# Optimization experiments

Measured on AMD Instinct MI355X. Metric: run time of the kernel, lower is better.

Reference implementation:

```python
import jax, jax.numpy as jnp
import numpy as np


def setup_inputs() -> dict:
    key = jax.random.key(0)
    k1, k2 = jax.random.split(key)
    return {
        "embeddings": jax.random.normal(k1, (4, 768, 32, 32), dtype=jnp.float32),
        "database": jax.random.normal(k2, (20000, 768), dtype=jnp.float32),
        "k": 3,
        "out_h": 512,
        "out_w": 512,
    }


def reference(embeddings, database, k, out_h, out_w):
    # embeddings: [B, D, h, w]  (segmenter hidden state), database: [N, D]
    B, D, h, w = embeddings.shape
    # B x h x w x D -> B x (h*w) x D query layout, as in _get_ood_scores
    q = jnp.transpose(embeddings, (0, 2, 3, 1)).reshape(B, h * w, D)
    # squared Euclidean distances via (||q||^2 + ||x||^2 - 2 q.x)
    q2 = jnp.sum(q * q, axis=-1)[..., None]                 # [B, hw, 1]
    x2 = jnp.sum(database * database, axis=-1)[None, None]  # [1, 1, N]
    d2 = q2 + x2 - 2.0 * jnp.einsum("bqd,nd->bqn", q, database)
    dist = jnp.sqrt(jnp.maximum(d2, 1e-12))                 # [B, hw, N]
    # k smallest distances (sklearn kneighbors) then mean over neighbors
    neg_topk, _ = jax.lax.top_k(-dist, k)                   # [B, hw, k]
    ood = jnp.mean(-neg_topk, axis=-1).reshape(B, h, w)
    # F.interpolate(..., mode='bilinear', align_corners=False) == half-pixel bilinear
    ood_up = jax.image.resize(ood[:, None], (B, 1, out_h, out_w), method="bilinear")
    return ood_up
```

## Files before the change

kernel.cpp:

```cpp
#include <hip/hip_runtime.h>
#include <hip/hip_bf16.h>
#include <math.h>

constexpr int B    = 4;
constexpr int D    = 768;
constexpr int HW   = 1024;
constexpr int M    = B * HW;
constexpr int NDB  = 20000;
constexpr int NDBP = 20096;
constexpr int OUTH = 512;
constexpr int OUTW = 512;

constexpr int BM     = 128;
constexpr int BN     = 128;
constexpr int KSTEPS = D / 64;
constexpr int GSTEPS = KSTEPS / 2;
constexpr int NSPLIT = 32;
constexpr int NT2    = 157;
constexpr int STEPB  = BM * 64;

typedef int   i32x8  __attribute__((ext_vector_type(8)));
typedef float f32x16 __attribute__((ext_vector_type(16)));

__device__ __forceinline__ void insert3(float& t0, float& t1, float& t2, float d) {
    float a0 = fminf(d, t0);
    float b0 = fmaxf(d, t0);
    float a1 = fminf(b0, t1);
    float b1 = fmaxf(b0, t1);
    t0 = a0; t1 = a1;
    t2 = fminf(b1, t2);
}

__device__ __forceinline__ unsigned int pack4_fp8(float a, float b, float c, float d) {
    int v = __builtin_amdgcn_cvt_pk_fp8_f32(a, b, 0, false);
    v = __builtin_amdgcn_cvt_pk_fp8_f32(c, d, v, true);
    return (unsigned int)v;
}

__device__ __forceinline__ void gl_lds16(const unsigned char* g, unsigned char* l) {
    __builtin_amdgcn_global_load_lds(
        (const __attribute__((address_space(1))) void*)g,
        (__attribute__((address_space(3))) void*)l, 16, 0, 0);
}

__global__ __launch_bounds__(256) void db_convert(const float* __restrict__ db,
                                                  uint4* __restrict__ dbt8,
                                                  float* __restrict__ x2p) {
    __shared__ float part[512];
    const int tile = blockIdx.x;
    const int g    = blockIdx.y;
    const int t    = threadIdx.x;
    const int n0   = tile * BM;

    #pragma unroll
    for (int pass = 0; pass < 2; ++pass) {
        int idx = pass * 256 + t;
        int r  = idx & 31;
        int kc = (idx >> 5) & 1;
        int h2 = (idx >> 6) & 1;
        int rg = idx >> 7;
        int row = rg * 32 + r;
        int n = n0 + row;
        int kb = g * 64 + kc * 32 + h2 * 16;
        float4 v0 = make_float4(0.f, 0.f, 0.f, 0.f), v1 = v0, v2 = v0, v3 = v0;
        if (n < NDB) {
            const float4* p = (const float4*)(db + (size_t)n * D + kb);
            v0 = p[0]; v1 = p[1]; v2 = p[2]; v3 = p[3];
        }
        float ss = v0.x*v0.x + v0.y*v0.y + v0.z*v0.z + v0.w*v0.w
                 + v1.x*v1.x + v1.y*v1.y + v1.z*v1.z + v1.w*v1.w
                 + v2.x*v2.x + v2.y*v2.y + v2.z*v2.z + v2.w*v2.w
                 + v3.x*v3.x + v3.y*v3.y + v3.z*v3.z + v3.w*v3.w;
        uint4 o;
        o.x = pack4_fp8(v0.x, v0.y, v0.z, v0.w);
        o.y = pack4_fp8(v1.x, v1.y, v1.z, v1.w);
        o.z = pack4_fp8(v2.x, v2.y, v2.z, v2.w);
        o.w = pack4_fp8(v3.x, v3.y, v3.z, v3.w);
        dbt8[((size_t)tile * KSTEPS + g) * 512 + idx] = o;
        part[idx] = ss;
    }
    __syncthreads();
    if (t < 128) {
        int rg = t >> 5, r = t & 31;
        int base = rg * 128 + r;
        float s = part[base] + part[base + 32] + part[base + 64] + part[base + 96];
        x2p[((size_t)tile * KSTEPS + g) * 128 + t] = s;
    }
}

__global__ __launch_bounds__(256) void x2_reduce(const float* __restrict__ x2p,
                                                 float* __restrict__ x2) {
    int n = blockIdx.x * 256 + threadIdx.x;
    if (n >= NDBP) return;
    if (n >= NDB) { x2[n] = 1e30f; return; }
    const float* p = x2p + (size_t)(n >> 7) * KSTEPS * 128 + (n & 127);
    float s = 0.f;
    #pragma unroll
    for (int g = 0; g < KSTEPS; ++g) s += p[g * 128];
    x2[n] = s;
}

__global__ __launch_bounds__(256) void q_convert(const float* __restrict__ emb,
                                                 uint4* __restrict__ qbt8,
                                                 float* __restrict__ q2p) {
    __shared__ float part[512];
    const int qt = blockIdx.x;
    const int g  = blockIdx.y;
    const int t  = threadIdx.x;
    const int b  = qt >> 3;
    const int p0 = (qt & 7) * 128;

    #pragma unroll
    for (int pass = 0; pass < 2; ++pass) {
        int idx = pass * 256 + t;
        int r  = idx & 31;
        int kc = (idx >> 5) & 1;
        int h2 = (idx >> 6) & 1;
        int rg = idx >> 7;
        int prow = rg * 32 + r;
        int kb = g * 64 + kc * 32 + h2 * 16;
        const float* src = emb + ((size_t)b * D + kb) * HW + p0 + prow;
        float v[16];
        float ss = 0.f;
        #pragma unroll
        for (int j = 0; j < 16; ++j) {
            v[j] = src[(size_t)j * HW];
            ss = fmaf(v[j], v[j], ss);
        }
        uint4 o;
        o.x = pack4_fp8(-2.f*v[0],  -2.f*v[1],  -2.f*v[2],  -2.f*v[3]);
        o.y = pack4_fp8(-2.f*v[4],  -2.f*v[5],  -2.f*v[6],  -2.f*v[7]);
        o.z = pack4_fp8(-2.f*v[8],  -2.f*v[9],  -2.f*v[10], -2.f*v[11]);
        o.w = pack4_fp8(-2.f*v[12], -2.f*v[13], -2.f*v[14], -2.f*v[15]);
        qbt8[((size_t)qt * KSTEPS + g) * 512 + idx] = o;
        part[idx] = ss;
    }
    __syncthreads();
    if (t < 128) {
        int rg = t >> 5, r = t & 31;
        int base = rg * 128 + r;
        float s = part[base] + part[base + 32] + part[base + 64] + part[base + 96];
        q2p[((size_t)qt * KSTEPS + g) * 128 + t] = s;
    }
}

__global__ __launch_bounds__(256, 4) void gemm_topk(const unsigned char* __restrict__ dbt8,
                                                    const unsigned char* __restrict__ qbt8,
                                                    const float* __restrict__ x2g,
                                                    float* __restrict__ partials) {
    __shared__ __align__(16) unsigned char As[2 * STEPB];
    __shared__ __align__(16) unsigned char Bs[2 * STEPB];
    __shared__ float X2s[BM];
    __shared__ float red[2][BN][3];

    const int tid  = threadIdx.x;
    const int lane = tid & 63;
    const int w    = tid >> 6;
    const int wr   = w >> 1, wc = w & 1;
    const int h    = lane >> 5;
    const int l31  = lane & 31;

    const int bid   = blockIdx.x;
    const int xcd   = bid & 7;
    const int j     = bid >> 3;
    const int sp    = xcd + 8 * (j >> 5);
    const int qtile = j & 31;
    const int m0    = qtile * BN;

    const int afrag = (wr * 2) * 2048 + h * 512 + l31 * 16;
    const int bfrag = (wc * 2) * 2048 + h * 512 + l31 * 16;

    const int lb = lane * 16;
    const unsigned char* qstep0 = qbt8 + (size_t)qtile * KSTEPS * STEPB + w * 2048 + lb;

    float t0[2], t1[2], t2[2];
    #pragma unroll
    for (int jj = 0; jj < 2; ++jj) { t0[jj] = INFINITY; t1[jj] = INFINITY; t2[jj] = INFINITY; }

    for (int tile = sp; tile < NT2; tile += NSPLIT) {
        const int n0 = tile * BM;
        const unsigned char* astep = dbt8 + (size_t)tile * KSTEPS * STEPB + w * 2048 + lb;
        const unsigned char* bstep = qstep0;

        f32x16 acc[2][2];
        #pragma unroll
        for (int i = 0; i < 2; ++i)
            #pragma unroll
            for (int jj = 0; jj < 2; ++jj)
                #pragma unroll
                for (int r = 0; r < 16; ++r) acc[i][jj][r] = 0.f;

        for (int g2 = 0; g2 < GSTEPS; ++g2) {
            __syncthreads();
            gl_lds16(astep,                As + w * 2048);
            gl_lds16(astep + 1024,         As + w * 2048 + 1024);
            gl_lds16(astep + STEPB,        As + 8192 + w * 2048);
            gl_lds16(astep + STEPB + 1024, As + 8192 + w * 2048 + 1024);
            gl_lds16(bstep,                Bs + w * 2048);
            gl_lds16(bstep + 1024,         Bs + w * 2048 + 1024);
            gl_lds16(bstep + STEPB,        Bs + 8192 + w * 2048);
            gl_lds16(bstep + STEPB + 1024, Bs + 8192 + w * 2048 + 1024);
            if (g2 == 0 && tid < BM) X2s[tid] = x2g[n0 + tid];
            astep += 2 * STEPB;
            bstep += 2 * STEPB;
            __syncthreads();

            #pragma unroll
            for (int s = 0; s < 2; ++s) {
                i32x8 af[2], bf[2];
                #pragma unroll
                for (int i = 0; i < 2; ++i) {
                    int4 lo = *(const int4*)(As + s * 8192 + afrag + i * 2048);
                    int4 hi = *(const int4*)(As + s * 8192 + afrag + i * 2048 + 1024);
                    af[i] = (i32x8){lo.x, lo.y, lo.z, lo.w, hi.x, hi.y, hi.z, hi.w};
                }
                #pragma unroll
                for (int jj = 0; jj < 2; ++jj) {
                    int4 lo = *(const int4*)(Bs + s * 8192 + bfrag + jj * 2048);
                    int4 hi = *(const int4*)(Bs + s * 8192 + bfrag + jj * 2048 + 1024);
                    bf[jj] = (i32x8){lo.x, lo.y, lo.z, lo.w, hi.x, hi.y, hi.z, hi.w};
                }
                #pragma unroll
                for (int i = 0; i < 2; ++i)
                    #pragma unroll
                    for (int jj = 0; jj < 2; ++jj)
                        acc[i][jj] = __builtin_amdgcn_mfma_scale_f32_32x32x64_f8f6f4(
                            af[i], bf[jj], acc[i][jj], 0, 0,
                            0, 0x7f7f7f7f, 0, 0x7f7f7f7f);
            }
        }

        #pragma unroll
        for (int i = 0; i < 2; ++i) {
            #pragma unroll
            for (int rg2 = 0; rg2 < 4; ++rg2) {
                float4 xv = *(const float4*)&X2s[wr * 64 + i * 32 + rg2 * 8 + 4 * h];
                #pragma unroll
                for (int jj = 0; jj < 2; ++jj) {
                    #pragma unroll
                    for (int rr = 0; rr < 4; ++rr) {
                        float s = acc[i][jj][rg2 * 4 + rr] + ((const float*)&xv)[rr];
                        insert3(t0[jj], t1[jj], t2[jj], s);
                    }
                }
            }
        }
    }

    #pragma unroll
    for (int jj = 0; jj < 2; ++jj) {
        float o0 = __shfl_xor(t0[jj], 32);
        float o1 = __shfl_xor(t1[jj], 32);
        float o2 = __shfl_xor(t2[jj], 32);
        insert3(t0[jj], t1[jj], t2[jj], o0);
        insert3(t0[jj], t1[jj], t2[jj], o1);
        insert3(t0[jj], t1[jj], t2[jj], o2);
    }
    if (h == 0) {
        #pragma unroll
        for (int jj = 0; jj < 2; ++jj) {
            int col = wc * 64 + jj * 32 + l31;
            red[wr][col][0] = t0[jj];
            red[wr][col][1] = t1[jj];
            red[wr][col][2] = t2[jj];
        }
    }
    __syncthreads();
    if (tid < BN) {
        float a0 = red[0][tid][0], a1 = red[0][tid][1], a2 = red[0][tid][2];
        insert3(a0, a1, a2, red[1][tid][0]);
        insert3(a0, a1, a2, red[1][tid][1]);
        insert3(a0, a1, a2, red[1][tid][2]);
        float* dst = partials + ((size_t)(m0 + tid) * NSPLIT + sp) * 3;
        dst[0] = a0; dst[1] = a1; dst[2] = a2;
    }
}

__global__ __launch_bounds__(256) void merge_ood(const float* __restrict__ partials,
                                                 const float* __restrict__ q2p,
                                                 float* __restrict__ ood) {
    int m = blockIdx.x * 256 + threadIdx.x;
    if (m >= M) return;
    const float* pp = partials + (size_t)m * NSPLIT * 3;
    float a0 = INFINITY, a1 = INFINITY, a2 = INFINITY;
    #pragma unroll
    for (int j = 0; j < NSPLIT * 3; ++j) insert3(a0, a1, a2, pp[j]);
    const float* qp = q2p + (size_t)(m >> 7) * KSTEPS * 128 + (m & 127);
    float q = 0.f;
    #pragma unroll
    for (int g = 0; g < KSTEPS; ++g) q += qp[g * 128];
    float d0 = sqrtf(fmaxf(q + a0, 1e-12f));
    float d1 = sqrtf(fmaxf(q + a1, 1e-12f));
    float d2 = sqrtf(fmaxf(q + a2, 1e-12f));
    ood[m] = (d0 + d1 + d2) * (1.f / 3.f);
}

__global__ __launch_bounds__(256) void upsample(const float* __restrict__ ood,
                                                float* __restrict__ out) {
    int idx = blockIdx.x * 256 + threadIdx.x;
    int ox = idx & (OUTW - 1);
    int oy = (idx >> 9) & (OUTH - 1);
    int bb = idx >> 18;
    float sx = (ox + 0.5f) * (32.f / OUTW) - 0.5f;
    float sy = (oy + 0.5f) * (32.f / OUTH) - 0.5f;
    float fx = floorf(sx), fy = floorf(sy);
    float wx = sx - fx, wy = sy - fy;
    int x0 = max(0, min(31, (int)fx));
    int x1 = max(0, min(31, (int)fx + 1));
    int y0 = max(0, min(31, (int)fy));
    int y1 = max(0, min(31, (int)fy + 1));
    const float* src = ood + bb * 1024;
    float v00 = src[y0 * 32 + x0];
    float v01 = src[y0 * 32 + x1];
    float v10 = src[y1 * 32 + x0];
    float v11 = src[y1 * 32 + x1];
    float top = v00 + wx * (v01 - v00);
    float bot = v10 + wx * (v11 - v10);
    out[idx] = top + wy * (bot - top);
}

extern "C" void kernel_launch(void* const* d_in, const int* in_sizes, int n_in,
                              void* d_out, int out_size, void* d_ws, size_t ws_size,
                              hipStream_t stream) {
    const float* emb = (const float*)d_in[0];
    const float* db  = (const float*)d_in[1];
    float* out = (float*)d_out;

    char* ws = (char*)d_ws;
    unsigned char* dbt8 = (unsigned char*)ws;
    unsigned char* qbt8 = (unsigned char*)(ws + 15433728);
    float* x2       = (float*)(ws + 18579456);
    float* x2p      = (float*)(ws + 18659840);
    float* q2p      = (float*)(ws + 19624448);
    float* ood      = (float*)(ws + 19821056);
    float* partials = (float*)(ws + 19837440);

    db_convert<<<dim3(NT2, KSTEPS), 256, 0, stream>>>(db, (uint4*)dbt8, x2p);
    q_convert<<<dim3(32, KSTEPS), 256, 0, stream>>>(emb, (uint4*)qbt8, q2p);
    x2_reduce<<<(NDBP + 255) / 256, 256, 0, stream>>>(x2p, x2);
    gemm_topk<<<NSPLIT * 32, 256, 0, stream>>>(dbt8, qbt8, x2, partials);
    merge_ood<<<(M + 255) / 256, 256, 0, stream>>>(partials, q2p, ood);
    upsample<<<(B * OUTH * OUTW) / 256, 256, 0, stream>>>(ood, out);
}
```

Measured before the change: 213.6 us.

## Enlarge GEMM database tile to 256 rows and stage db conversion through LDS

```diff
diff --git a/kernel.cpp b/kernel.cpp
--- a/kernel.cpp
+++ b/kernel.cpp
@@ -7,17 +7,18 @@
 constexpr int HW   = 1024;
 constexpr int M    = B * HW;
 constexpr int NDB  = 20000;
-constexpr int NDBP = 20096;
+constexpr int LT   = 158;
+constexpr int NDBP = LT * 128;
 constexpr int OUTH = 512;
 constexpr int OUTW = 512;
 
-constexpr int BM     = 128;
+constexpr int BM     = 256;
 constexpr int BN     = 128;
 constexpr int KSTEPS = D / 64;
 constexpr int GSTEPS = KSTEPS / 2;
-constexpr int NSPLIT = 32;
-constexpr int NT2    = 157;
-constexpr int STEPB  = BM * 64;
+constexpr int NSPLIT = 16;
+constexpr int NT2    = 79;
+constexpr int STEPB  = 128 * 64;
 
 typedef int   i32x8  __attribute__((ext_vector_type(8)));
 typedef float f32x16 __attribute__((ext_vector_type(16)));
@@ -46,12 +47,26 @@
 __global__ __launch_bounds__(256) void db_convert(const float* __restrict__ db,
                                                   uint4* __restrict__ dbt8,
                                                   float* __restrict__ x2p) {
+    __shared__ float panel[128][65];
     __shared__ float part[512];
-    const int tile = blockIdx.x;
-    const int g    = blockIdx.y;
-    const int t    = threadIdx.x;
-    const int n0   = tile * BM;
-
+    const int lt = blockIdx.x;
+    const int g  = blockIdx.y;
+    const int t  = threadIdx.x;
+    const int n0 = lt * 128;
+
+    #pragma unroll
+    for (int pass = 0; pass < 8; ++pass) {
+        int idx = pass * 256 + t;
+        int row = idx >> 4, c4 = idx & 15;
+        int n = n0 + row;
+        float4 v = make_float4(0.f, 0.f, 0.f, 0.f);
+        if (n < NDB) v = *(const float4*)(db + (size_t)n * D + g * 64 + c4 * 4);
+        panel[row][c4 * 4 + 0] = v.x;
+        panel[row][c4 * 4 + 1] = v.y;
+        panel[row][c4 * 4 + 2] = v.z;
+        panel[row][c4 * 4 + 3] = v.w;
+    }
+    __syncthreads();
     #pragma unroll
     for (int pass = 0; pass < 2; ++pass) {
         int idx = pass * 256 + t;
@@ -59,32 +74,28 @@
         int kc = (idx >> 5) & 1;
         int h2 = (idx >> 6) & 1;
         int rg = idx >> 7;
-        int row = rg * 32 + r;
-        int n = n0 + row;
-        int kb = g * 64 + kc * 32 + h2 * 16;
-        float4 v0 = make_float4(0.f, 0.f, 0.f, 0.f), v1 = v0, v2 = v0, v3 = v0;
-        if (n < NDB) {
-            const float4* p = (const float4*)(db + (size_t)n * D + kb);
-            v0 = p[0]; v1 = p[1]; v2 = p[2]; v3 = p[3];
-        }
-        float ss = v0.x*v0.x + v0.y*v0.y + v0.z*v0.z + v0.w*v0.w
-                 + v1.x*v1.x + v1.y*v1.y + v1.z*v1.z + v1.w*v1.w
-                 + v2.x*v2.x + v2.y*v2.y + v2.z*v2.z + v2.w*v2.w
-                 + v3.x*v3.x + v3.y*v3.y + v3.z*v3.z + v3.w*v3.w;
+        int row  = rg * 32 + r;
+        int kloc = kc * 32 + h2 * 16;
+        float v[16];
+        float ss = 0.f;
+        #pragma unroll
+        for (int j = 0; j < 16; ++j) {
+            v[j] = panel[row][kloc + j];
+            ss = fmaf(v[j], v[j], ss);
+        }
         uint4 o;
-        o.x = pack4_fp8(v0.x, v0.y, v0.z, v0.w);
-        o.y = pack4_fp8(v1.x, v1.y, v1.z, v1.w);
-        o.z = pack4_fp8(v2.x, v2.y, v2.z, v2.w);
-        o.w = pack4_fp8(v3.x, v3.y, v3.z, v3.w);
-        dbt8[((size_t)tile * KSTEPS + g) * 512 + idx] = o;
+        o.x = pack4_fp8(v[0],  v[1],  v[2],  v[3]);
+        o.y = pack4_fp8(v[4],  v[5],  v[6],  v[7]);
+        o.z = pack4_fp8(v[8],  v[9],  v[10], v[11]);
+        o.w = pack4_fp8(v[12], v[13], v[14], v[15]);
+        dbt8[((size_t)lt * KSTEPS + g) * 512 + idx] = o;
         part[idx] = ss;
     }
     __syncthreads();
     if (t < 128) {
-        int rg = t >> 5, r = t & 31;
-        int base = rg * 128 + r;
+        int base = (t >> 5) * 128 + (t & 31);
         float s = part[base] + part[base + 32] + part[base + 64] + part[base + 96];
-        x2p[((size_t)tile * KSTEPS + g) * 128 + t] = s;
+        x2p[((size_t)lt * KSTEPS + g) * 128 + t] = s;
     }
 }
 
@@ -137,26 +148,26 @@
     }
     __syncthreads();
     if (t < 128) {
-        int rg = t >> 5, r = t & 31;
-        int base = rg * 128 + r;
+        int base = (t >> 5) * 128 + (t & 31);
         float s = part[base] + part[base + 32] + part[base + 64] + part[base + 96];
         q2p[((size_t)qt * KSTEPS + g) * 128 + t] = s;
     }
 }
 
-__global__ __launch_bounds__(256, 4) void gemm_topk(const unsigned char* __restrict__ dbt8,
+__global__ __launch_bounds__(256, 2) void gemm_topk(const unsigned char* __restrict__ dbt8,
                                                     const unsigned char* __restrict__ qbt8,
                                                     const float* __restrict__ x2g,
                                                     float* __restrict__ partials) {
-    __shared__ __align__(16) unsigned char As[2 * STEPB];
+    __shared__ __align__(16) unsigned char As[4 * STEPB];
     __shared__ __align__(16) unsigned char Bs[2 * STEPB];
     __shared__ float X2s[BM];
-    __shared__ float red[2][BN][3];
+    __shared__ float red[4][BN][3];
 
     const int tid  = threadIdx.x;
     const int lane = tid & 63;
     const int w    = tid >> 6;
-    const int wr   = w >> 1, wc = w & 1;
+    const int lts  = w >> 1;
+    const int wr   = w & 1;
     const int h    = lane >> 5;
     const int l31  = lane & 31;
 
@@ -167,65 +178,66 @@
     const int qtile = j & 31;
     const int m0    = qtile * BN;
 
-    const int afrag = (wr * 2) * 2048 + h * 512 + l31 * 16;
-    const int bfrag = (wc * 2) * 2048 + h * 512 + l31 * 16;
+    int a_off[2], b_off[4];
+    #pragma unroll
+    for (int i = 0; i < 2; ++i) a_off[i] = lts * 16384 + (wr * 2 + i) * 2048 + h * 512 + l31 * 16;
+    #pragma unroll
+    for (int j4 = 0; j4 < 4; ++j4) b_off[j4] = j4 * 2048 + h * 512 + l31 * 16;
 
     const int lb = lane * 16;
-    const unsigned char* qstep0 = qbt8 + (size_t)qtile * KSTEPS * STEPB + w * 2048 + lb;
-
-    float t0[2], t1[2], t2[2];
-    #pragma unroll
-    for (int jj = 0; jj < 2; ++jj) { t0[jj] = INFINITY; t1[jj] = INFINITY; t2[jj] = INFINITY; }
+    const unsigned char* qstep0 = qbt8 + ((size_t)qtile * KSTEPS + lts) * STEPB + wr * 4096 + lb;
+    unsigned char* bdst = Bs + lts * 8192 + wr * 4096;
+    unsigned char* adst = As + w * 8192;
+
+    float t0[4], t1[4], t2[4];
+    #pragma unroll
+    for (int j4 = 0; j4 < 4; ++j4) { t0[j4] = INFINITY; t1[j4] = INFINITY; t2[j4] = INFINITY; }
 
     for (int tile = sp; tile < NT2; tile += NSPLIT) {
         const int n0 = tile * BM;
-        const unsigned char* astep = dbt8 + (size_t)tile * KSTEPS * STEPB + w * 2048 + lb;
+        const unsigned char* astep = dbt8 + (((size_t)(2 * tile + lts) * KSTEPS) + wr) * STEPB + lb;
         const unsigned char* bstep = qstep0;
 
-        f32x16 acc[2][2];
+        f32x16 acc[2][4];
         #pragma unroll
         for (int i = 0; i < 2; ++i)
             #pragma unroll
-            for (int jj = 0; jj < 2; ++jj)
-                #pragma unroll
-                for (int r = 0; r < 16; ++r) acc[i][jj][r] = 0.f;
+            for (int j4 = 0; j4 < 4; ++j4)
+                #pragma unroll
+                for (int r = 0; r < 16; ++r) acc[i][j4][r] = 0.f;
 
         for (int g2 = 0; g2 < GSTEPS; ++g2) {
             __syncthreads();
-            gl_lds16(astep,                As + w * 2048);
-            gl_lds16(astep + 1024,         As + w * 2048 + 1024);
-            gl_lds16(astep + STEPB,        As + 8192 + w * 2048);
-            gl_lds16(astep + STEPB + 1024, As + 8192 + w * 2048 + 1024);
-            gl_lds16(bstep,                Bs + w * 2048);
-            gl_lds16(bstep + 1024,         Bs + w * 2048 + 1024);
-            gl_lds16(bstep + STEPB,        Bs + 8192 + w * 2048);
-            gl_lds16(bstep + STEPB + 1024, Bs + 8192 + w * 2048 + 1024);
-            if (g2 == 0 && tid < BM) X2s[tid] = x2g[n0 + tid];
+            #pragma unroll
+            for (int l = 0; l < 8; ++l) gl_lds16(astep + l * 1024, adst + l * 1024);
+            #pragma unroll
+            for (int l = 0; l < 4; ++l) gl_lds16(bstep + l * 1024, bdst + l * 1024);
+            if (g2 == 0) X2s[tid] = x2g[n0 + tid];
             astep += 2 * STEPB;
             bstep += 2 * STEPB;
             __syncthreads();
 
             #pragma unroll
             for (int s = 0; s < 2; ++s) {
-                i32x8 af[2], bf[2];
+                i32x8 af[2], bf[4];
                 #pragma unroll
                 for (int i = 0; i < 2; ++i) {
-                    int4 lo = *(const int4*)(As + s * 8192 + afrag + i * 2048);
-                    int4 hi = *(const int4*)(As + s * 8192 + afrag + i * 2048 + 1024);
+                    int4 lo = *(const int4*)(As + s * 8192 + a_off[i]);
+                    int4 hi = *(const int4*)(As + s * 8192 + a_off[i] + 1024);
                     af[i] = (i32x8){lo.x, lo.y, lo.z, lo.w, hi.x, hi.y, hi.z, hi.w};
                 }
                 #pragma unroll
-                for (int jj = 0; jj < 2; ++jj) {
-                    int4 lo = *(const int4*)(Bs + s * 8192 + bfrag + jj * 2048);
-                    int4 hi = *(const int4*)(Bs + s * 8192 + bfrag + jj * 2048 + 1024);
-                    bf[jj] = (i32x8){lo.x, lo.y, lo.z, lo.w, hi.x, hi.y, hi.z, hi.w};
+                for (int j4 = 0; j4 < 4; ++j4) {
+                    int4 lo = *(const int4*)(Bs + s * 8192 + b_off[j4]);
+                    int4 hi = *(const int4*)(Bs + s * 8192 + b_off[j4] + 1024);
+                    bf[j4] = (i32x8){lo.x, lo.y, lo.z, lo.w, hi.x, hi.y, hi.z, hi.w};
                 }
                 #pragma unroll
                 for (int i = 0; i < 2; ++i)
                     #pragma unroll
-                    for (int jj = 0; jj < 2; ++jj)
-                        acc[i][jj] = __builtin_amdgcn_mfma_scale_f32_32x32x64_f8f6f4(
-                            af[i], bf[jj], acc[i][jj], 0, 0,
+                    for (int j4 = 0; j4 < 4; ++j4)
+                        acc[i][j4] = __builtin_amdgcn_mfma_scale_f32_32x32x64_f8f6f4(
+                            af[i], bf[j4], acc[i][j4], 0, 0,
                             0, 0x7f7f7f7f, 0, 0x7f7f7f7f);
             }
         }
@@ -234,13 +246,13 @@
         for (int i = 0; i < 2; ++i) {
             #pragma unroll
             for (int rg2 = 0; rg2 < 4; ++rg2) {
-                float4 xv = *(const float4*)&X2s[wr * 64 + i * 32 + rg2 * 8 + 4 * h];
-                #pragma unroll
-                for (int jj = 0; jj < 2; ++jj) {
+                float4 xv = *(const float4*)&X2s[w * 64 + i * 32 + rg2 * 8 + 4 * h];
+                #pragma unroll
+                for (int j4 = 0; j4 < 4; ++j4) {
                     #pragma unroll
                     for (int rr = 0; rr < 4; ++rr) {
-                        float s = acc[i][jj][rg2 * 4 + rr] + ((const float*)&xv)[rr];
-                        insert3(t0[jj], t1[jj], t2[jj], s);
+                        float s = acc[i][j4][rg2 * 4 + rr] + ((const float*)&xv)[rr];
+                        insert3(t0[j4], t1[j4], t2[j4], s);
                     }
                 }
             }
@@ -248,29 +260,32 @@
     }
 
     #pragma unroll
-    for (int jj = 0; jj < 2; ++jj) {
-        float o0 = __shfl_xor(t0[jj], 32);
-        float o1 = __shfl_xor(t1[jj], 32);
-        float o2 = __shfl_xor(t2[jj], 32);
-        insert3(t0[jj], t1[jj], t2[jj], o0);
-        insert3(t0[jj], t1[jj], t2[jj], o1);
-        insert3(t0[jj], t1[jj], t2[jj], o2);
+    for (int j4 = 0; j4 < 4; ++j4) {
+        float o0 = __shfl_xor(t0[j4], 32);
+        float o1 = __shfl_xor(t1[j4], 32);
+        float o2 = __shfl_xor(t2[j4], 32);
+        insert3(t0[j4], t1[j4], t2[j4], o0);
+        insert3(t0[j4], t1[j4], t2[j4], o1);
+        insert3(t0[j4], t1[j4], t2[j4], o2);
     }
     if (h == 0) {
         #pragma unroll
-        for (int jj = 0; jj < 2; ++jj) {
-            int col = wc * 64 + jj * 32 + l31;
-            red[wr][col][0] = t0[jj];
-            red[wr][col][1] = t1[jj];
-            red[wr][col][2] = t2[jj];
+        for (int j4 = 0; j4 < 4; ++j4) {
+            int col = j4 * 32 + l31;
+            red[w][col][0] = t0[j4];
+            red[w][col][1] = t1[j4];
+            red[w][col][2] = t2[j4];
         }
     }
     __syncthreads();
     if (tid < BN) {
         float a0 = red[0][tid][0], a1 = red[0][tid][1], a2 = red[0][tid][2];
-        insert3(a0, a1, a2, red[1][tid][0]);
-        insert3(a0, a1, a2, red[1][tid][1]);
-        insert3(a0, a1, a2, red[1][tid][2]);
+        #pragma unroll
+        for (int ww = 1; ww < 4; ++ww) {
+            insert3(a0, a1, a2, red[ww][tid][0]);
+            insert3(a0, a1, a2, red[ww][tid][1]);
+            insert3(a0, a1, a2, red[ww][tid][2]);
+        }
         float* dst = partials + ((size_t)(m0 + tid) * NSPLIT + sp) * 3;
         dst[0] = a0; dst[1] = a1; dst[2] = a2;
     }
@@ -328,14 +343,14 @@
 
     char* ws = (char*)d_ws;
     unsigned char* dbt8 = (unsigned char*)ws;
-    unsigned char* qbt8 = (unsigned char*)(ws + 15433728);
-    float* x2       = (float*)(ws + 18579456);
-    float* x2p      = (float*)(ws + 18659840);
-    float* q2p      = (float*)(ws + 19624448);
-    float* ood      = (float*)(ws + 19821056);
-    float* partials = (float*)(ws + 19837440);
-
-    db_convert<<<dim3(NT2, KSTEPS), 256, 0, stream>>>(db, (uint4*)dbt8, x2p);
+    unsigned char* qbt8 = (unsigned char*)(ws + 15532032);
+    float* x2       = (float*)(ws + 18677760);
+    float* x2p      = (float*)(ws + 18758656);
+    float* q2p      = (float*)(ws + 19729408);
+    float* ood      = (float*)(ws + 19926016);
+    float* partials = (float*)(ws + 19942400);
+
+    db_convert<<<dim3(LT, KSTEPS), 256, 0, stream>>>(db, (uint4*)dbt8, x2p);
     q_convert<<<dim3(32, KSTEPS), 256, 0, stream>>>(emb, (uint4*)qbt8, q2p);
     x2_reduce<<<(NDBP + 255) / 256, 256, 0, stream>>>(x2p, x2);
     gemm_topk<<<NSPLIT * 32, 256, 0, stream>>>(dbt8, qbt8, x2, partials);
```

Measured after the change: 184.4 us. 1.16x faster.
